# Optimization experiments

Hardware: AMD Instinct MI355X
Metric: run time of the kernel (lower is better)

The kernel has to match this reference:

```python
import jax, jax.numpy as jnp
import numpy as np

TEMPERATURE = 5.0

def setup_inputs() -> dict:
    key = jax.random.key(0)
    k1, k2 = jax.random.split(key)
    B, D = 8192, 128
    features = jax.random.normal(k1, (B, D), dtype=jnp.float32)
    labels = jax.random.randint(k2, (B,), 0, 100, dtype=jnp.int64)
    return {"features": features, "labels": labels, "fac_label": 3}


def reference(features, labels, fac_label):
    # features: [B, D], labels: [B]
    B = features.shape[0]
    # positive-pair mask; note original's mask_scale row-copy loop is a no-op,
    # so mask_scale == mask, and mask_cross_feature == ones (fac_label unused in effect)
    mask = (labels[:, None] == labels[None, :]).astype(features.dtype)  # [B, B]

    sim = jnp.matmul(features, features.T) / TEMPERATURE  # [B, B]
    logits_max = jax.lax.stop_gradient(jnp.max(sim, axis=1, keepdims=True))
    logits = sim - logits_max

    # remove self-contrast (diagonal)
    logits_mask = 1.0 - jnp.eye(B, dtype=features.dtype)
    mask = mask * logits_mask

    exp_logits = jnp.exp(logits) * logits_mask
    log_prob = logits - jnp.log(1e-12 + exp_logits.sum(axis=1, keepdims=True))

    mean_log_prob_pos_mask = (mask * log_prob).sum(axis=1)  # [B]
    # vectorized form of the per-element reciprocal loop: 1/count where count>0 else 0
    cnt = mask.sum(axis=1)
    recip = jnp.where(cnt == 0, 0.0, 1.0 / jnp.where(cnt == 0, 1.0, cnt))

    loss = -(mean_log_prob_pos_mask * recip).mean()
    return loss
```

## Files before the change

kernel.cpp:

```cpp
#include <hip/hip_runtime.h>


#define BN 8192
#define DK 128
#define INV_T 0.2f
#define C1F 0.28853901f
#define C40F 27.7258872f

#define TILES 1056
#define PSLOTS 64

#define NCLS 100
#define PB 128
#define PROWS (BN / PB)

#define FBLKS 128

#define OFF_FB    0
#define OFF_PART  (2 * 1024 * 1024)
#define OFF_G     (OFF_PART + PSLOTS * BN * 4)
#define OFF_HIST  (OFF_G + NCLS * DK * 4)
#define OFF_BSUM  (OFF_HIST + 512)
#define OFF_CTR   (OFF_BSUM + 1024)

typedef __attribute__((ext_vector_type(8))) short bf16x8;
typedef __attribute__((ext_vector_type(4))) float f32x4;

__device__ __forceinline__ unsigned short f2bf(float f) {
    unsigned u = __builtin_bit_cast(unsigned, f);
    u += 0x7fffu + ((u >> 16) & 1u);
    return (unsigned short)(u >> 16);
}

__device__ __forceinline__ float fexp2(float x) {
#if __has_builtin(__builtin_amdgcn_exp2f)
    return __builtin_amdgcn_exp2f(x);
#else
    float r; asm("v_exp_f32 %0, %1" : "=v"(r) : "v"(x)); return r;
#endif
}

__device__ __forceinline__ void load_lds16(const void* g, void* l) {
    __builtin_amdgcn_global_load_lds(
        (const __attribute__((address_space(1))) unsigned int*)g,
        (__attribute__((address_space(3))) unsigned int*)l, 16, 0, 0);
}

__global__ __launch_bounds__(256) void prep_kernel(const float* __restrict__ F,
                                                   unsigned short* __restrict__ Fb,
                                                   float* __restrict__ part,
                                                   unsigned int* __restrict__ ctr) {
    const int t = threadIdx.x;
    const int b = blockIdx.x;

    if (b == 0 && t == 0) *ctr = 0u;

    {
        float4* pz = (float4*)(part + (size_t)32 * BN) + (size_t)b * 512;
        pz[t]       = make_float4(0.f, 0.f, 0.f, 0.f);
        pz[t + 256] = make_float4(0.f, 0.f, 0.f, 0.f);
    }

    const float4* F4  = (const float4*)F + (size_t)b * (PROWS * DK / 4);
    ushort4*      Fb4 = (ushort4*)Fb + (size_t)b * (PROWS * DK / 4);
#pragma unroll
    for (int k = 0; k < PROWS * DK / 4 / 256; ++k) {
        float4 v = F4[k * 256 + t];
        ushort4 o;
        o.x = f2bf(v.x); o.y = f2bf(v.y); o.z = f2bf(v.z); o.w = f2bf(v.w);
        Fb4[k * 256 + t] = o;
    }
}

template <bool DIAGT>
__device__ __forceinline__ void supcon_tile(const short* __restrict__ Fb,
                                            float* __restrict__ part,
                                            int bx, int cy, char* smem) {
    const int t    = threadIdx.x;
    const int wave = t >> 6, lane = t & 63;
    const int quad = lane >> 4, l16 = lane & 15;
    const int rowBase = bx * 128 + wave * 32;
    const int colBase = cy * 256;

    const char* Btile = (const char*)Fb + (size_t)colBase * 256;
    const int   gso   = (t & 15) * 256 + (t >> 6) * 64 + ((t >> 4) & 3) * 16;
    char*       ldsw  = smem + wave * 1024;

#pragma unroll
    for (int tt = 0; tt < 4; ++tt)
        load_lds16(Btile + tt * 4096 + gso, ldsw + tt * 4096);

    bf16x8 a[2][4];
#pragma unroll
    for (int rt = 0; rt < 2; ++rt)
#pragma unroll
        for (int kt = 0; kt < 4; ++kt)
            a[rt][kt] = *(const bf16x8*)(Fb + (size_t)(rowBase + rt * 16 + l16) * DK
                                            + kt * 32 + quad * 8);

    float Zs[2][4];
#pragma unroll
    for (int rt = 0; rt < 2; ++rt)
#pragma unroll
        for (int r = 0; r < 4; ++r) Zs[rt][r] = 0.f;
    float Zcol[4];

    const int    roffb   = quad * 256 + l16 * 16;
    float* const colpart = part + (size_t)(32 + (bx >> 1)) * BN + colBase;

    __syncthreads();

#pragma unroll
    for (int g = 0; g < 4; ++g) {
        if (g < 3) {
            char* dsth = smem + ((g + 1) & 1) * 16384 + wave * 1024;
#pragma unroll
            for (int tt = 0; tt < 4; ++tt)
                load_lds16(Btile + (size_t)((g + 1) * 4 + tt) * 4096 + gso,
                           dsth + tt * 4096);
        }
        const char* srch = smem + (g & 1) * 16384;
#pragma unroll
        for (int tt = 0; tt < 4; ++tt) {
            const int jt = g * 4 + tt;
            bf16x8 bb[4];
#pragma unroll
            for (int kt = 0; kt < 4; ++kt)
                bb[kt] = *(const bf16x8*)(srch + tt * 4096 + kt * 1024 + roffb);
            float Zc0 = 0.f, Zc1 = 0.f;
#pragma unroll
            for (int rt = 0; rt < 2; ++rt) {
                f32x4 acc = {0.f, 0.f, 0.f, 0.f};
#pragma unroll
                for (int kt = 0; kt < 4; ++kt)
                    acc = __builtin_amdgcn_mfma_f32_16x16x32_bf16(a[rt][kt], bb[kt],
                                                                  acc, 0, 0, 0);
#pragma unroll
                for (int r = 0; r < 4; ++r) {
                    float e = fexp2(fmaf(acc[r], C1F, -40.0f));
                    if (DIAGT) {
                        if (colBase + jt * 16 + l16 == rowBase + rt * 16 + quad * 4 + r)
                            e = 0.f;
                    }
                    Zs[rt][r] += e;
                    if (!DIAGT) { if (rt == 0) Zc0 += e; else Zc1 += e; }
                }
            }
            if (!DIAGT) {
                float Zc = Zc0 + Zc1;
                Zc += __shfl_xor(Zc, 16);
                Zc += __shfl_xor(Zc, 32);
                Zcol[tt] = Zc;
            }
        }
        if (g < 3) __syncthreads();
        if (!DIAGT && quad == 0) {
#pragma unroll
            for (int tt = 0; tt < 4; ++tt)
                atomicAdd(colpart + (g * 4 + tt) * 16 + l16, Zcol[tt]);
        }
    }

#pragma unroll
    for (int rt = 0; rt < 2; ++rt)
#pragma unroll
        for (int r = 0; r < 4; ++r) {
            float zz = Zs[rt][r];
#pragma unroll
            for (int h = 1; h < 16; h <<= 1) zz += __shfl_xor(zz, h);
            if (l16 == 0)
                part[(size_t)cy * BN + rowBase + rt * 16 + quad * 4 + r] = zz;
        }
}

__device__ __forceinline__ void class_rider(const float* __restrict__ F,
                                            const int* __restrict__ labels,
                                            float* __restrict__ G,
                                            int* __restrict__ hist,
                                            int c, char* smem) {
    const int t    = threadIdx.x;
    int*      rows = (int*)smem;
    int*      nrs  = (int*)(smem + 8192);
    float*    gh   = (float*)(smem + 8192 + 64);

    if (t == 0) *nrs = 0;
    __syncthreads();
#pragma unroll
    for (int k = 0; k < BN / 256; ++k) {
        const int r = k * 256 + t;
        if (labels[r] == c) {
            const int idx = atomicAdd(nrs, 1);
            if (idx < 2048) rows[idx] = r;
        }
    }
    __syncthreads();
    const int n = *nrs;

    const int half = t >> 7, col = t & 127;
    float acc = 0.f;
    for (int j = half; j < n; j += 2)
        acc += F[(size_t)rows[j] * DK + col];
    gh[t] = acc;
    __syncthreads();
    if (t < DK) G[c * DK + t] = gh[t] + gh[t + DK];
    if (t == 0) hist[c] = n;
}

__global__ __launch_bounds__(256) void supcon_main(const short* __restrict__ Fb,
                                                   float* __restrict__ part,
                                                   const float* __restrict__ F,
                                                   const int* __restrict__ labels,
                                                   float* __restrict__ G,
                                                   int* __restrict__ hist) {
    __shared__ alignas(16) char smem[32768];
    const int bid = blockIdx.x;
    if (bid >= TILES) {
        class_rider(F, labels, G, hist, bid - TILES, smem);
        return;
    }
    int k0 = (int)sqrtf((float)bid);
    while ((k0 + 1) * (k0 + 1) <= bid) ++k0;
    while (k0 * k0 > bid) --k0;
    int bx, cy;
    if (bid < k0 * k0 + k0) { bx = 2 * k0 - 1; cy = bid - k0 * k0; }
    else                    { bx = 2 * k0;     cy = bid - k0 * k0 - k0; }
    if (cy == (bx >> 1)) supcon_tile<true >(Fb, part, bx, cy, smem);
    else                 supcon_tile<false>(Fb, part, bx, cy, smem);
}

__global__ __launch_bounds__(64) void supcon_finalize(const float* __restrict__ F,
                                                      const int* __restrict__ labels,
                                                      const float* __restrict__ part,
                                                      const float* __restrict__ G,
                                                      const int* __restrict__ hist,
                                                      float* __restrict__ bsums,
                                                      unsigned int* __restrict__ ctr,
                                                      float* __restrict__ out) {
    const int t  = threadIdx.x;
    const int i  = blockIdx.x * 64 + t;
    const int c2 = blockIdx.x >> 2;

    float Zm = 0.f;
#pragma unroll 8
    for (int k = 0; k < 32; ++k) {
        const int slot = (k <= c2) ? k : 32 + k;
        Zm += part[(size_t)slot * BN + i];
    }

    const int   lbl = labels[i];
    const float cnt = (float)(hist[lbl] - 1);

    const float4* fr = (const float4*)(F + (size_t)i * DK);
    const float4* gr = (const float4*)(G + lbl * DK);
    float dot = 0.f, nrm = 0.f;
#pragma unroll 8
    for (int k = 0; k < DK / 4; ++k) {
        const float4 av = fr[k], gv = gr[k];
        dot += av.x * gv.x + av.y * gv.y + av.z * gv.z + av.w * gv.w;
        nrm += av.x * av.x + av.y * av.y + av.z * av.z + av.w * av.w;
    }

    const float mt = nrm * INV_T;
    const float A  = (dot - nrm) * INV_T;
    float term = 0.f;
    if (cnt > 0.5f)
        term = (A - cnt * mt) / cnt - __logf(1e-12f + Zm * __expf(C40F - mt));

    float sum = term;
#pragma unroll
    for (int h = 1; h < 64; h <<= 1) sum += __shfl_xor(sum, h);

    __shared__ int lastf;
    if (t == 0) {
        bsums[blockIdx.x] = sum;
        __threadfence();
        const unsigned old = atomicAdd(ctr, 1u);
        lastf = (old == FBLKS - 1);
    }
    __syncthreads();
    if (lastf) {
        const volatile float* vb = bsums;
        float v = vb[t] + vb[t + 64];
#pragma unroll
        for (int h = 1; h < 64; h <<= 1) v += __shfl_xor(v, h);
        if (t == 0) out[0] = -v * (1.0f / BN);
    }
}

extern "C" void kernel_launch(void* const* d_in, const int* in_sizes, int n_in,
                              void* d_out, int out_size, void* d_ws, size_t ws_size,
                              hipStream_t stream) {
    const float* F      = (const float*)d_in[0];
    const int*   labels = (const int*)d_in[1];
    float* out = (float*)d_out;
    char*  ws  = (char*)d_ws;

    unsigned short* Fb    = (unsigned short*)(ws + OFF_FB);
    float*          part  = (float*)(ws + OFF_PART);
    float*          G     = (float*)(ws + OFF_G);
    int*            hist  = (int*)(ws + OFF_HIST);
    float*          bsums = (float*)(ws + OFF_BSUM);
    unsigned int*   ctr   = (unsigned int*)(ws + OFF_CTR);

    prep_kernel<<<PB, 256, 0, stream>>>(F, Fb, part, ctr);
    supcon_main<<<TILES + NCLS, 256, 0, stream>>>((const short*)Fb, part,
                                                  F, labels, G, hist);
    supcon_finalize<<<FBLKS, 64, 0, stream>>>(F, labels, part, G, hist,
                                              bsums, ctr, out);
}
```

Measured before the change: 121.6 us.

## Load B tiles directly from global to registers and move class sums to prep

Drops the LDS double-buffered async global-to-LDS staging of the column (B) tile in the main tile kernel. Each wave now reads its bf16 operand fragments straight from global memory into registers, with software prefetch of the next 16-column slab. Column atomics are issued per 16-column step instead of batched per group. The per-class feature summation blocks move from the main kernel's grid into the prep kernel's grid, so the main kernel uses no shared memory and has no barriers, at the cost of redundant global/L2 reads across the four waves.

```diff
diff --git a/kernel.cpp b/kernel.cpp
--- a/kernel.cpp
+++ b/kernel.cpp
@@ -40,18 +40,49 @@
 #endif
 }
 
-__device__ __forceinline__ void load_lds16(const void* g, void* l) {
-    __builtin_amdgcn_global_load_lds(
-        (const __attribute__((address_space(1))) unsigned int*)g,
-        (__attribute__((address_space(3))) unsigned int*)l, 16, 0, 0);
+__device__ __forceinline__ void class_rider(const float* __restrict__ F,
+                                            const int* __restrict__ labels,
+                                            float* __restrict__ G,
+                                            int* __restrict__ hist, int c) {
+    const int t = threadIdx.x;
+    __shared__ int   rows[2048];
+    __shared__ int   nrs;
+    __shared__ float gh[256];
+
+    if (t == 0) nrs = 0;
+    __syncthreads();
+#pragma unroll
+    for (int k = 0; k < BN / 256; ++k) {
+        const int r = k * 256 + t;
+        if (labels[r] == c) {
+            const int idx = atomicAdd(&nrs, 1);
+            if (idx < 2048) rows[idx] = r;
+        }
+    }
+    __syncthreads();
+    const int n = nrs;
+
+    const int half = t >> 7, col = t & 127;
+    float acc = 0.f;
+    for (int j = half; j < n; j += 2)
+        acc += F[(size_t)rows[j] * DK + col];
+    gh[t] = acc;
+    __syncthreads();
+    if (t < DK) G[c * DK + t] = gh[t] + gh[t + DK];
+    if (t == 0) hist[c] = n;
 }
 
 __global__ __launch_bounds__(256) void prep_kernel(const float* __restrict__ F,
+                                                   const int* __restrict__ labels,
                                                    unsigned short* __restrict__ Fb,
                                                    float* __restrict__ part,
+                                                   float* __restrict__ G,
+                                                   int* __restrict__ hist,
                                                    unsigned int* __restrict__ ctr) {
     const int t = threadIdx.x;
     const int b = blockIdx.x;
+
+    if (b >= PB) { class_rider(F, labels, G, hist, b - PB); return; }
 
     if (b == 0 && t == 0) *ctr = 0u;
 
@@ -75,21 +106,13 @@
 template <bool DIAGT>
 __device__ __forceinline__ void supcon_tile(const short* __restrict__ Fb,
                                             float* __restrict__ part,
-                                            int bx, int cy, char* smem) {
+                                            int bx, int cy) {
     const int t    = threadIdx.x;
     const int wave = t >> 6, lane = t & 63;
     const int quad = lane >> 4, l16 = lane & 15;
     const int rowBase = bx * 128 + wave * 32;
     const int colBase = cy * 256;
 
-    const char* Btile = (const char*)Fb + (size_t)colBase * 256;
-    const int   gso   = (t & 15) * 256 + (t >> 6) * 64 + ((t >> 4) & 3) * 16;
-    char*       ldsw  = smem + wave * 1024;
-
-#pragma unroll
-    for (int tt = 0; tt < 4; ++tt)
-        load_lds16(Btile + tt * 4096 + gso, ldsw + tt * 4096);
-
     bf16x8 a[2][4];
 #pragma unroll
     for (int rt = 0; rt < 2; ++rt)
@@ -103,62 +126,52 @@
     for (int rt = 0; rt < 2; ++rt)
 #pragma unroll
         for (int r = 0; r < 4; ++r) Zs[rt][r] = 0.f;
-    float Zcol[4];
-
-    const int    roffb   = quad * 256 + l16 * 16;
+
     float* const colpart = part + (size_t)(32 + (bx >> 1)) * BN + colBase;
 
-    __syncthreads();
-
-#pragma unroll
-    for (int g = 0; g < 4; ++g) {
-        if (g < 3) {
-            char* dsth = smem + ((g + 1) & 1) * 16384 + wave * 1024;
-#pragma unroll
-            for (int tt = 0; tt < 4; ++tt)
-                load_lds16(Btile + (size_t)((g + 1) * 4 + tt) * 4096 + gso,
-                           dsth + tt * 4096);
-        }
-        const char* srch = smem + (g & 1) * 16384;
-#pragma unroll
-        for (int tt = 0; tt < 4; ++tt) {
-            const int jt = g * 4 + tt;
-            bf16x8 bb[4];
+    const short* bp = Fb + (size_t)(colBase + l16) * DK + quad * 8;
+    bf16x8 bc[4], bn[4];
+#pragma unroll
+    for (int kt = 0; kt < 4; ++kt) bc[kt] = *(const bf16x8*)(bp + kt * 32);
+
+    auto STEP = [&](const bf16x8 (&bb)[4], int jt) {
+        float Zc = 0.f;
+#pragma unroll
+        for (int rt = 0; rt < 2; ++rt) {
+            f32x4 acc = {0.f, 0.f, 0.f, 0.f};
 #pragma unroll
             for (int kt = 0; kt < 4; ++kt)
-                bb[kt] = *(const bf16x8*)(srch + tt * 4096 + kt * 1024 + roffb);
-            float Zc0 = 0.f, Zc1 = 0.f;
-#pragma unroll
-            for (int rt = 0; rt < 2; ++rt) {
-                f32x4 acc = {0.f, 0.f, 0.f, 0.f};
-#pragma unroll
-                for (int kt = 0; kt < 4; ++kt)
-                    acc = __builtin_amdgcn_mfma_f32_16x16x32_bf16(a[rt][kt], bb[kt],
-                                                                  acc, 0, 0, 0);
-#pragma unroll
-                for (int r = 0; r < 4; ++r) {
-                    float e = fexp2(fmaf(acc[r], C1F, -40.0f));
-                    if (DIAGT) {
-                        if (colBase + jt * 16 + l16 == rowBase + rt * 16 + quad * 4 + r)
-                            e = 0.f;
-                    }
-                    Zs[rt][r] += e;
-                    if (!DIAGT) { if (rt == 0) Zc0 += e; else Zc1 += e; }
+                acc = __builtin_amdgcn_mfma_f32_16x16x32_bf16(a[rt][kt], bb[kt],
+                                                              acc, 0, 0, 0);
+#pragma unroll
+            for (int r = 0; r < 4; ++r) {
+                float e = fexp2(fmaf(acc[r], C1F, -40.0f));
+                if (DIAGT) {
+                    if (colBase + jt * 16 + l16 == rowBase + rt * 16 + quad * 4 + r)
+                        e = 0.f;
                 }
+                Zs[rt][r] += e;
+                if (!DIAGT) Zc += e;
             }
-            if (!DIAGT) {
-                float Zc = Zc0 + Zc1;
-                Zc += __shfl_xor(Zc, 16);
-                Zc += __shfl_xor(Zc, 32);
-                Zcol[tt] = Zc;
-            }
-        }
-        if (g < 3) __syncthreads();
-        if (!DIAGT && quad == 0) {
-#pragma unroll
-            for (int tt = 0; tt < 4; ++tt)
-                atomicAdd(colpart + (g * 4 + tt) * 16 + l16, Zcol[tt]);
-        }
+        }
+        if (!DIAGT) {
+            Zc += __shfl_xor(Zc, 16);
+            Zc += __shfl_xor(Zc, 32);
+            if (quad == 0) atomicAdd(colpart + jt * 16 + l16, Zc);
+        }
+    };
+
+    for (int jt = 0; jt < 16; jt += 2) {
+        bp += 16 * DK;
+#pragma unroll
+        for (int kt = 0; kt < 4; ++kt) bn[kt] = *(const bf16x8*)(bp + kt * 32);
+        STEP(bc, jt);
+        if (jt + 2 < 16) {
+            bp += 16 * DK;
+#pragma unroll
+            for (int kt = 0; kt < 4; ++kt) bc[kt] = *(const bf16x8*)(bp + kt * 32);
+        }
+        STEP(bn, jt + 1);
     }
 
 #pragma unroll
@@ -173,59 +186,17 @@
         }
 }
 
-__device__ __forceinline__ void class_rider(const float* __restrict__ F,
-                                            const int* __restrict__ labels,
-                                            float* __restrict__ G,
-                                            int* __restrict__ hist,
-                                            int c, char* smem) {
-    const int t    = threadIdx.x;
-    int*      rows = (int*)smem;
-    int*      nrs  = (int*)(smem + 8192);
-    float*    gh   = (float*)(smem + 8192 + 64);
-
-    if (t == 0) *nrs = 0;
-    __syncthreads();
-#pragma unroll
-    for (int k = 0; k < BN / 256; ++k) {
-        const int r = k * 256 + t;
-        if (labels[r] == c) {
-            const int idx = atomicAdd(nrs, 1);
-            if (idx < 2048) rows[idx] = r;
-        }
-    }
-    __syncthreads();
-    const int n = *nrs;
-
-    const int half = t >> 7, col = t & 127;
-    float acc = 0.f;
-    for (int j = half; j < n; j += 2)
-        acc += F[(size_t)rows[j] * DK + col];
-    gh[t] = acc;
-    __syncthreads();
-    if (t < DK) G[c * DK + t] = gh[t] + gh[t + DK];
-    if (t == 0) hist[c] = n;
-}
-
 __global__ __launch_bounds__(256) void supcon_main(const short* __restrict__ Fb,
-                                                   float* __restrict__ part,
-                                                   const float* __restrict__ F,
-                                                   const int* __restrict__ labels,
-                                                   float* __restrict__ G,
-                                                   int* __restrict__ hist) {
-    __shared__ alignas(16) char smem[32768];
+                                                   float* __restrict__ part) {
     const int bid = blockIdx.x;
-    if (bid >= TILES) {
-        class_rider(F, labels, G, hist, bid - TILES, smem);
-        return;
-    }
     int k0 = (int)sqrtf((float)bid);
     while ((k0 + 1) * (k0 + 1) <= bid) ++k0;
     while (k0 * k0 > bid) --k0;
     int bx, cy;
     if (bid < k0 * k0 + k0) { bx = 2 * k0 - 1; cy = bid - k0 * k0; }
     else                    { bx = 2 * k0;     cy = bid - k0 * k0 - k0; }
-    if (cy == (bx >> 1)) supcon_tile<true >(Fb, part, bx, cy, smem);
-    else                 supcon_tile<false>(Fb, part, bx, cy, smem);
+    if (cy == (bx >> 1)) supcon_tile<true >(Fb, part, bx, cy);
+    else                 supcon_tile<false>(Fb, part, bx, cy);
 }
 
 __global__ __launch_bounds__(64) void supcon_finalize(const float* __restrict__ F,
@@ -302,9 +273,8 @@
     float*          bsums = (float*)(ws + OFF_BSUM);
     unsigned int*   ctr   = (unsigned int*)(ws + OFF_CTR);
 
-    prep_kernel<<<PB, 256, 0, stream>>>(F, Fb, part, ctr);
-    supcon_main<<<TILES + NCLS, 256, 0, stream>>>((const short*)Fb, part,
-                                                  F, labels, G, hist);
+    prep_kernel<<<PB + NCLS, 256, 0, stream>>>(F, labels, Fb, part, G, hist, ctr);
+    supcon_main<<<TILES, 256, 0, stream>>>((const short*)Fb, part);
     supcon_finalize<<<FBLKS, 64, 0, stream>>>(F, labels, part, G, hist,
                                               bsums, ctr, out);
 }
```

Result: slower. 136.3 us (+12.0%).

## Replace global column atomics with per-tile LDS reduction records

Applied to the files above, without the earlier changes.

Column partial sums of exp values were previously accumulated with global atomicAdd into zeroed slots. Each off-diagonal tile now reduces its column sums across waves in LDS and writes one 256-float record per tile. The finalize kernel gathers the records for each row by tile index, and the zeroing pass in prep is dropped. This removes atomic contention and traffic but adds an LDS barrier, a larger workspace and more scattered reads in finalize; launch bounds now also request 2 blocks per CU.

```diff
diff --git a/kernel.cpp b/kernel.cpp
--- a/kernel.cpp
+++ b/kernel.cpp
@@ -8,17 +8,15 @@
 #define C40F 27.7258872f
 
 #define TILES 1056
-#define PSLOTS 64
-
 #define NCLS 100
 #define PB 128
 #define PROWS (BN / PB)
-
 #define FBLKS 128
 
 #define OFF_FB    0
 #define OFF_PART  (2 * 1024 * 1024)
-#define OFF_G     (OFF_PART + PSLOTS * BN * 4)
+#define OFF_CREC  (OFF_PART + 32 * BN * 4)
+#define OFF_G     (OFF_CREC + TILES * 256 * 4)
 #define OFF_HIST  (OFF_G + NCLS * DK * 4)
 #define OFF_BSUM  (OFF_HIST + 512)
 #define OFF_CTR   (OFF_BSUM + 1024)
@@ -48,18 +46,10 @@
 
 __global__ __launch_bounds__(256) void prep_kernel(const float* __restrict__ F,
                                                    unsigned short* __restrict__ Fb,
-                                                   float* __restrict__ part,
                                                    unsigned int* __restrict__ ctr) {
     const int t = threadIdx.x;
     const int b = blockIdx.x;
-
     if (b == 0 && t == 0) *ctr = 0u;
-
-    {
-        float4* pz = (float4*)(part + (size_t)32 * BN) + (size_t)b * 512;
-        pz[t]       = make_float4(0.f, 0.f, 0.f, 0.f);
-        pz[t + 256] = make_float4(0.f, 0.f, 0.f, 0.f);
-    }
 
     const float4* F4  = (const float4*)F + (size_t)b * (PROWS * DK / 4);
     ushort4*      Fb4 = (ushort4*)Fb + (size_t)b * (PROWS * DK / 4);
@@ -72,15 +62,50 @@
     }
 }
 
+__device__ __forceinline__ void class_rider(const float* __restrict__ F,
+                                            const int* __restrict__ labels,
+                                            float* __restrict__ G,
+                                            int* __restrict__ hist,
+                                            int c, char* smem) {
+    const int t    = threadIdx.x;
+    int*      rows = (int*)smem;
+    int*      nrs  = (int*)(smem + 8192);
+    float*    gh   = (float*)(smem + 8192 + 64);
+
+    if (t == 0) *nrs = 0;
+    __syncthreads();
+#pragma unroll
+    for (int k = 0; k < BN / 256; ++k) {
+        const int r = k * 256 + t;
+        if (labels[r] == c) {
+            const int idx = atomicAdd(nrs, 1);
+            if (idx < 2048) rows[idx] = r;
+        }
+    }
+    __syncthreads();
+    const int n = *nrs;
+
+    const int half = t >> 7, col = t & 127;
+    float acc = 0.f;
+    for (int j = half; j < n; j += 2)
+        acc += F[(size_t)rows[j] * DK + col];
+    gh[t] = acc;
+    __syncthreads();
+    if (t < DK) G[c * DK + t] = gh[t] + gh[t + DK];
+    if (t == 0) hist[c] = n;
+}
+
 template <bool DIAGT>
 __device__ __forceinline__ void supcon_tile(const short* __restrict__ Fb,
                                             float* __restrict__ part,
-                                            int bx, int cy, char* smem) {
+                                            float* __restrict__ crec,
+                                            int bx, int cy, int bid, char* smem) {
     const int t    = threadIdx.x;
     const int wave = t >> 6, lane = t & 63;
     const int quad = lane >> 4, l16 = lane & 15;
     const int rowBase = bx * 128 + wave * 32;
     const int colBase = cy * 256;
+    float*    colred  = (float*)(smem + 32768);
 
     const char* Btile = (const char*)Fb + (size_t)colBase * 256;
     const int   gso   = (t & 15) * 256 + (t >> 6) * 64 + ((t >> 4) & 3) * 16;
@@ -103,10 +128,8 @@
     for (int rt = 0; rt < 2; ++rt)
 #pragma unroll
         for (int r = 0; r < 4; ++r) Zs[rt][r] = 0.f;
-    float Zcol[4];
-
-    const int    roffb   = quad * 256 + l16 * 16;
-    float* const colpart = part + (size_t)(32 + (bx >> 1)) * BN + colBase;
+
+    const int roffb = quad * 256 + l16 * 16;
 
     __syncthreads();
 
@@ -150,15 +173,10 @@
                 float Zc = Zc0 + Zc1;
                 Zc += __shfl_xor(Zc, 16);
                 Zc += __shfl_xor(Zc, 32);
-                Zcol[tt] = Zc;
+                if (quad == 0) colred[wave * 256 + jt * 16 + l16] = Zc;
             }
         }
         if (g < 3) __syncthreads();
-        if (!DIAGT && quad == 0) {
-#pragma unroll
-            for (int tt = 0; tt < 4; ++tt)
-                atomicAdd(colpart + (g * 4 + tt) * 16 + l16, Zcol[tt]);
-        }
     }
 
 #pragma unroll
@@ -171,48 +189,22 @@
             if (l16 == 0)
                 part[(size_t)cy * BN + rowBase + rt * 16 + quad * 4 + r] = zz;
         }
-}
-
-__device__ __forceinline__ void class_rider(const float* __restrict__ F,
-                                            const int* __restrict__ labels,
-                                            float* __restrict__ G,
-                                            int* __restrict__ hist,
-                                            int c, char* smem) {
-    const int t    = threadIdx.x;
-    int*      rows = (int*)smem;
-    int*      nrs  = (int*)(smem + 8192);
-    float*    gh   = (float*)(smem + 8192 + 64);
-
-    if (t == 0) *nrs = 0;
-    __syncthreads();
-#pragma unroll
-    for (int k = 0; k < BN / 256; ++k) {
-        const int r = k * 256 + t;
-        if (labels[r] == c) {
-            const int idx = atomicAdd(nrs, 1);
-            if (idx < 2048) rows[idx] = r;
-        }
-    }
-    __syncthreads();
-    const int n = *nrs;
-
-    const int half = t >> 7, col = t & 127;
-    float acc = 0.f;
-    for (int j = half; j < n; j += 2)
-        acc += F[(size_t)rows[j] * DK + col];
-    gh[t] = acc;
-    __syncthreads();
-    if (t < DK) G[c * DK + t] = gh[t] + gh[t + DK];
-    if (t == 0) hist[c] = n;
-}
-
-__global__ __launch_bounds__(256) void supcon_main(const short* __restrict__ Fb,
-                                                   float* __restrict__ part,
-                                                   const float* __restrict__ F,
-                                                   const int* __restrict__ labels,
-                                                   float* __restrict__ G,
-                                                   int* __restrict__ hist) {
-    __shared__ alignas(16) char smem[32768];
+
+    if (!DIAGT) {
+        __syncthreads();
+        crec[(size_t)bid * 256 + t] =
+            colred[t] + colred[256 + t] + colred[512 + t] + colred[768 + t];
+    }
+}
+
+__global__ __launch_bounds__(256, 2) void supcon_main(const short* __restrict__ Fb,
+                                                      float* __restrict__ part,
+                                                      float* __restrict__ crec,
+                                                      const float* __restrict__ F,
+                                                      const int* __restrict__ labels,
+                                                      float* __restrict__ G,
+                                                      int* __restrict__ hist) {
+    __shared__ alignas(16) char smem[36864];
     const int bid = blockIdx.x;
     if (bid >= TILES) {
         class_rider(F, labels, G, hist, bid - TILES, smem);
@@ -224,13 +216,14 @@
     int bx, cy;
     if (bid < k0 * k0 + k0) { bx = 2 * k0 - 1; cy = bid - k0 * k0; }
     else                    { bx = 2 * k0;     cy = bid - k0 * k0 - k0; }
-    if (cy == (bx >> 1)) supcon_tile<true >(Fb, part, bx, cy, smem);
-    else                 supcon_tile<false>(Fb, part, bx, cy, smem);
+    if (cy == (bx >> 1)) supcon_tile<true >(Fb, part, crec, bx, cy, bid, smem);
+    else                 supcon_tile<false>(Fb, part, crec, bx, cy, bid, smem);
 }
 
 __global__ __launch_bounds__(64) void supcon_finalize(const float* __restrict__ F,
                                                       const int* __restrict__ labels,
                                                       const float* __restrict__ part,
+                                                      const float* __restrict__ crec,
                                                       const float* __restrict__ G,
                                                       const int* __restrict__ hist,
                                                       float* __restrict__ bsums,
@@ -239,12 +232,13 @@
     const int t  = threadIdx.x;
     const int i  = blockIdx.x * 64 + t;
     const int c2 = blockIdx.x >> 2;
+    const int cl = i & 255;
 
     float Zm = 0.f;
-#pragma unroll 8
-    for (int k = 0; k < 32; ++k) {
-        const int slot = (k <= c2) ? k : 32 + k;
-        Zm += part[(size_t)slot * BN + i];
+    for (int k = 0; k <= c2; ++k) Zm += part[(size_t)k * BN + i];
+    for (int k = c2 + 1; k < 32; ++k) {
+        Zm += crec[(size_t)(k * k + k + c2) * 256 + cl];
+        Zm += crec[(size_t)((k + 1) * (k + 1) + c2) * 256 + cl];
     }
 
     const int   lbl = labels[i];
@@ -297,14 +291,15 @@
 
     unsigned short* Fb    = (unsigned short*)(ws + OFF_FB);
     float*          part  = (float*)(ws + OFF_PART);
+    float*          crec  = (float*)(ws + OFF_CREC);
     float*          G     = (float*)(ws + OFF_G);
     int*            hist  = (int*)(ws + OFF_HIST);
     float*          bsums = (float*)(ws + OFF_BSUM);
     unsigned int*   ctr   = (unsigned int*)(ws + OFF_CTR);
 
-    prep_kernel<<<PB, 256, 0, stream>>>(F, Fb, part, ctr);
-    supcon_main<<<TILES + NCLS, 256, 0, stream>>>((const short*)Fb, part,
+    prep_kernel<<<PB, 256, 0, stream>>>(F, Fb, ctr);
+    supcon_main<<<TILES + NCLS, 256, 0, stream>>>((const short*)Fb, part, crec,
                                                   F, labels, G, hist);
-    supcon_finalize<<<FBLKS, 64, 0, stream>>>(F, labels, part, G, hist,
+    supcon_finalize<<<FBLKS, 64, 0, stream>>>(F, labels, part, crec, G, hist,
                                               bsums, ctr, out);
 }
```

New measurement: 117.6 us. 3.3% less time.

## Compute full similarity matrix instead of symmetric triangle with atomic column sums

Applied to the files above, without the earlier changes.

Replaces the triangular tiling, which used symmetry and atomically accumulated column partial sums, with a full square tiling of 128-row by 512-column blocks that only produce row sums. This removes the atomics, the zeroing of partial slots in the prep kernel, and the sqrt-based tile index decoding, and it simplifies the finalize reduction to 16 chunks. In exchange it roughly doubles the matmul and exponential work. It also adds an occupancy hint to the launch bounds.

```diff
diff --git a/kernel.cpp b/kernel.cpp
--- a/kernel.cpp
+++ b/kernel.cpp
@@ -7,18 +7,21 @@
 #define C1F 0.28853901f
 #define C40F 27.7258872f
 
-#define TILES 1056
-#define PSLOTS 64
+#define CHUNKS 16
+#define CCOLS (BN / CHUNKS)
+#define NJT (CCOLS / 16)
+#define NGRP (NJT / 4)
+#define RPB 128
+#define TBLKS (BN / RPB * CHUNKS)
 
 #define NCLS 100
 #define PB 128
 #define PROWS (BN / PB)
-
 #define FBLKS 128
 
 #define OFF_FB    0
 #define OFF_PART  (2 * 1024 * 1024)
-#define OFF_G     (OFF_PART + PSLOTS * BN * 4)
+#define OFF_G     (OFF_PART + CHUNKS * BN * 4)
 #define OFF_HIST  (OFF_G + NCLS * DK * 4)
 #define OFF_BSUM  (OFF_HIST + 512)
 #define OFF_CTR   (OFF_BSUM + 1024)
@@ -48,18 +51,10 @@
 
 __global__ __launch_bounds__(256) void prep_kernel(const float* __restrict__ F,
                                                    unsigned short* __restrict__ Fb,
-                                                   float* __restrict__ part,
                                                    unsigned int* __restrict__ ctr) {
     const int t = threadIdx.x;
     const int b = blockIdx.x;
-
     if (b == 0 && t == 0) *ctr = 0u;
-
-    {
-        float4* pz = (float4*)(part + (size_t)32 * BN) + (size_t)b * 512;
-        pz[t]       = make_float4(0.f, 0.f, 0.f, 0.f);
-        pz[t + 256] = make_float4(0.f, 0.f, 0.f, 0.f);
-    }
 
     const float4* F4  = (const float4*)F + (size_t)b * (PROWS * DK / 4);
     ushort4*      Fb4 = (ushort4*)Fb + (size_t)b * (PROWS * DK / 4);
@@ -70,107 +65,6 @@
         o.x = f2bf(v.x); o.y = f2bf(v.y); o.z = f2bf(v.z); o.w = f2bf(v.w);
         Fb4[k * 256 + t] = o;
     }
-}
-
-template <bool DIAGT>
-__device__ __forceinline__ void supcon_tile(const short* __restrict__ Fb,
-                                            float* __restrict__ part,
-                                            int bx, int cy, char* smem) {
-    const int t    = threadIdx.x;
-    const int wave = t >> 6, lane = t & 63;
-    const int quad = lane >> 4, l16 = lane & 15;
-    const int rowBase = bx * 128 + wave * 32;
-    const int colBase = cy * 256;
-
-    const char* Btile = (const char*)Fb + (size_t)colBase * 256;
-    const int   gso   = (t & 15) * 256 + (t >> 6) * 64 + ((t >> 4) & 3) * 16;
-    char*       ldsw  = smem + wave * 1024;
-
-#pragma unroll
-    for (int tt = 0; tt < 4; ++tt)
-        load_lds16(Btile + tt * 4096 + gso, ldsw + tt * 4096);
-
-    bf16x8 a[2][4];
-#pragma unroll
-    for (int rt = 0; rt < 2; ++rt)
-#pragma unroll
-        for (int kt = 0; kt < 4; ++kt)
-            a[rt][kt] = *(const bf16x8*)(Fb + (size_t)(rowBase + rt * 16 + l16) * DK
-                                            + kt * 32 + quad * 8);
-
-    float Zs[2][4];
-#pragma unroll
-    for (int rt = 0; rt < 2; ++rt)
-#pragma unroll
-        for (int r = 0; r < 4; ++r) Zs[rt][r] = 0.f;
-    float Zcol[4];
-
-    const int    roffb   = quad * 256 + l16 * 16;
-    float* const colpart = part + (size_t)(32 + (bx >> 1)) * BN + colBase;
-
-    __syncthreads();
-
-#pragma unroll
-    for (int g = 0; g < 4; ++g) {
-        if (g < 3) {
-            char* dsth = smem + ((g + 1) & 1) * 16384 + wave * 1024;
-#pragma unroll
-            for (int tt = 0; tt < 4; ++tt)
-                load_lds16(Btile + (size_t)((g + 1) * 4 + tt) * 4096 + gso,
-                           dsth + tt * 4096);
-        }
-        const char* srch = smem + (g & 1) * 16384;
-#pragma unroll
-        for (int tt = 0; tt < 4; ++tt) {
-            const int jt = g * 4 + tt;
-            bf16x8 bb[4];
-#pragma unroll
-            for (int kt = 0; kt < 4; ++kt)
-                bb[kt] = *(const bf16x8*)(srch + tt * 4096 + kt * 1024 + roffb);
-            float Zc0 = 0.f, Zc1 = 0.f;
-#pragma unroll
-            for (int rt = 0; rt < 2; ++rt) {
-                f32x4 acc = {0.f, 0.f, 0.f, 0.f};
-#pragma unroll
-                for (int kt = 0; kt < 4; ++kt)
-                    acc = __builtin_amdgcn_mfma_f32_16x16x32_bf16(a[rt][kt], bb[kt],
-                                                                  acc, 0, 0, 0);
-#pragma unroll
-                for (int r = 0; r < 4; ++r) {
-                    float e = fexp2(fmaf(acc[r], C1F, -40.0f));
-                    if (DIAGT) {
-                        if (colBase + jt * 16 + l16 == rowBase + rt * 16 + quad * 4 + r)
-                            e = 0.f;
-                    }
-                    Zs[rt][r] += e;
-                    if (!DIAGT) { if (rt == 0) Zc0 += e; else Zc1 += e; }
-                }
-            }
-            if (!DIAGT) {
-                float Zc = Zc0 + Zc1;
-                Zc += __shfl_xor(Zc, 16);
-                Zc += __shfl_xor(Zc, 32);
-                Zcol[tt] = Zc;
-            }
-        }
-        if (g < 3) __syncthreads();
-        if (!DIAGT && quad == 0) {
-#pragma unroll
-            for (int tt = 0; tt < 4; ++tt)
-                atomicAdd(colpart + (g * 4 + tt) * 16 + l16, Zcol[tt]);
-        }
-    }
-
-#pragma unroll
-    for (int rt = 0; rt < 2; ++rt)
-#pragma unroll
-        for (int r = 0; r < 4; ++r) {
-            float zz = Zs[rt][r];
-#pragma unroll
-            for (int h = 1; h < 16; h <<= 1) zz += __shfl_xor(zz, h);
-            if (l16 == 0)
-                part[(size_t)cy * BN + rowBase + rt * 16 + quad * 4 + r] = zz;
-        }
 }
 
 __device__ __forceinline__ void class_rider(const float* __restrict__ F,
@@ -206,25 +100,106 @@
     if (t == 0) hist[c] = n;
 }
 
-__global__ __launch_bounds__(256) void supcon_main(const short* __restrict__ Fb,
-                                                   float* __restrict__ part,
-                                                   const float* __restrict__ F,
-                                                   const int* __restrict__ labels,
-                                                   float* __restrict__ G,
-                                                   int* __restrict__ hist) {
+template <bool DIAGT>
+__device__ __forceinline__ void supcon_tile(const short* __restrict__ Fb,
+                                            float* __restrict__ part,
+                                            int bx, int cy, char* smem) {
+    const int t    = threadIdx.x;
+    const int wave = t >> 6, lane = t & 63;
+    const int quad = lane >> 4, l16 = lane & 15;
+    const int rowBase = bx * RPB + wave * 32;
+    const int colBase = cy * CCOLS;
+
+    const char* Btile = (const char*)Fb + (size_t)colBase * 256;
+    const int   gso   = (t & 15) * 256 + (t >> 6) * 64 + ((t >> 4) & 3) * 16;
+    char*       ldsw  = smem + wave * 1024;
+
+#pragma unroll
+    for (int tt = 0; tt < 4; ++tt)
+        load_lds16(Btile + tt * 4096 + gso, ldsw + tt * 4096);
+
+    bf16x8 a[2][4];
+#pragma unroll
+    for (int rt = 0; rt < 2; ++rt)
+#pragma unroll
+        for (int kt = 0; kt < 4; ++kt)
+            a[rt][kt] = *(const bf16x8*)(Fb + (size_t)(rowBase + rt * 16 + l16) * DK
+                                            + kt * 32 + quad * 8);
+
+    float Zs[2][4];
+#pragma unroll
+    for (int rt = 0; rt < 2; ++rt)
+#pragma unroll
+        for (int r = 0; r < 4; ++r) Zs[rt][r] = 0.f;
+
+    const int roffb = quad * 256 + l16 * 16;
+
+    __syncthreads();
+
+    for (int g = 0; g < NGRP; ++g) {
+        if (g < NGRP - 1) {
+            char* dsth = smem + ((g + 1) & 1) * 16384 + wave * 1024;
+#pragma unroll
+            for (int tt = 0; tt < 4; ++tt)
+                load_lds16(Btile + (size_t)((g + 1) * 4 + tt) * 4096 + gso,
+                           dsth + tt * 4096);
+        }
+        const char* srch = smem + (g & 1) * 16384;
+#pragma unroll
+        for (int tt = 0; tt < 4; ++tt) {
+            const int jt = g * 4 + tt;
+            bf16x8 bb[4];
+#pragma unroll
+            for (int kt = 0; kt < 4; ++kt)
+                bb[kt] = *(const bf16x8*)(srch + tt * 4096 + kt * 1024 + roffb);
+#pragma unroll
+            for (int rt = 0; rt < 2; ++rt) {
+                f32x4 acc = {0.f, 0.f, 0.f, 0.f};
+#pragma unroll
+                for (int kt = 0; kt < 4; ++kt)
+                    acc = __builtin_amdgcn_mfma_f32_16x16x32_bf16(a[rt][kt], bb[kt],
+                                                                  acc, 0, 0, 0);
+#pragma unroll
+                for (int r = 0; r < 4; ++r) {
+                    float e = fexp2(fmaf(acc[r], C1F, -40.0f));
+                    if (DIAGT) {
+                        if (colBase + jt * 16 + l16 == rowBase + rt * 16 + quad * 4 + r)
+                            e = 0.f;
+                    }
+                    Zs[rt][r] += e;
+                }
+            }
+        }
+        if (g < NGRP - 1) __syncthreads();
+    }
+
+#pragma unroll
+    for (int rt = 0; rt < 2; ++rt)
+#pragma unroll
+        for (int r = 0; r < 4; ++r) {
+            float zz = Zs[rt][r];
+#pragma unroll
+            for (int h = 1; h < 16; h <<= 1) zz += __shfl_xor(zz, h);
+            if (l16 == 0)
+                part[(size_t)cy * BN + rowBase + rt * 16 + quad * 4 + r] = zz;
+        }
+}
+
+__global__ __launch_bounds__(256, 4) void supcon_main(const short* __restrict__ Fb,
+                                                      float* __restrict__ part,
+                                                      const float* __restrict__ F,
+                                                      const int* __restrict__ labels,
+                                                      float* __restrict__ G,
+                                                      int* __restrict__ hist) {
     __shared__ alignas(16) char smem[32768];
     const int bid = blockIdx.x;
-    if (bid >= TILES) {
-        class_rider(F, labels, G, hist, bid - TILES, smem);
+    if (bid >= TBLKS) {
+        class_rider(F, labels, G, hist, bid - TBLKS, smem);
         return;
     }
-    int k0 = (int)sqrtf((float)bid);
-    while ((k0 + 1) * (k0 + 1) <= bid) ++k0;
-    while (k0 * k0 > bid) --k0;
-    int bx, cy;
-    if (bid < k0 * k0 + k0) { bx = 2 * k0 - 1; cy = bid - k0 * k0; }
-    else                    { bx = 2 * k0;     cy = bid - k0 * k0 - k0; }
-    if (cy == (bx >> 1)) supcon_tile<true >(Fb, part, bx, cy, smem);
+    const int bx = bid >> 4;
+    const int cy = bid & 15;
+    if (cy == (bx >> 2)) supcon_tile<true >(Fb, part, bx, cy, smem);
     else                 supcon_tile<false>(Fb, part, bx, cy, smem);
 }
 
@@ -236,16 +211,12 @@
                                                       float* __restrict__ bsums,
                                                       unsigned int* __restrict__ ctr,
                                                       float* __restrict__ out) {
-    const int t  = threadIdx.x;
-    const int i  = blockIdx.x * 64 + t;
-    const int c2 = blockIdx.x >> 2;
+    const int t = threadIdx.x;
+    const int i = blockIdx.x * 64 + t;
 
     float Zm = 0.f;
-#pragma unroll 8
-    for (int k = 0; k < 32; ++k) {
-        const int slot = (k <= c2) ? k : 32 + k;
-        Zm += part[(size_t)slot * BN + i];
-    }
+#pragma unroll
+    for (int c = 0; c < CHUNKS; ++c) Zm += part[(size_t)c * BN + i];
 
     const int   lbl = labels[i];
     const float cnt = (float)(hist[lbl] - 1);
@@ -302,8 +273,8 @@
     float*          bsums = (float*)(ws + OFF_BSUM);
     unsigned int*   ctr   = (unsigned int*)(ws + OFF_CTR);
 
-    prep_kernel<<<PB, 256, 0, stream>>>(F, Fb, part, ctr);
-    supcon_main<<<TILES + NCLS, 256, 0, stream>>>((const short*)Fb, part,
+    prep_kernel<<<PB, 256, 0, stream>>>(F, Fb, ctr);
+    supcon_main<<<TBLKS + NCLS, 256, 0, stream>>>((const short*)Fb, part,
                                                   F, labels, G, hist);
     supcon_finalize<<<FBLKS, 64, 0, stream>>>(F, labels, part, G, hist,
                                               bsums, ctr, out);
```

New measurement: 149.6 us. 1.23x slower.
